# Kernel tuning notes

Hardware: AMD Instinct MI355X
Metric: run time of the kernel (lower is better)

## Reference

```python
import jax, jax.numpy as jnp
import numpy as np
from jax import lax

B, DIM, H, W = 32, 64, 1, 8192
HEADS = 8
EPS_LN = 1e-5
EPS_NORM = 1e-12


def setup_inputs() -> dict:
    key = jax.random.key(0)
    ks = jax.random.split(key, 20)
    g = lambda i, shape, s=0.05: jax.random.normal(ks[i], shape, jnp.float32) * s
    return dict(
        x=jax.random.normal(ks[0], (B, DIM, H, W), jnp.float32),
        qkv_w=g(1, (3 * DIM, DIM)), qkv_b=g(2, (3 * DIM,)),
        dw_w=g(3, (3 * DIM, 1, 3, 3)), dw_b=g(4, (3 * DIM,)),
        proj_w=g(5, (DIM, DIM)), proj_b=g(6, (DIM,)),
        temperature=jnp.ones((HEADS, 1, 1), jnp.float32),
        sp_w=g(7, (DIM,)), sp_b=g(8, (1,)),
        up_w=g(9, (3,)), up_b=g(10, (3,)),
        c2_w=g(11, (1, 1, 2)), c2_b=g(11, (1,)), ln2_w=jnp.ones((W,), jnp.float32), ln2_b=jnp.zeros((W,), jnp.float32),
        c4_w=g(12, (1, 1, 4)), c4_b=g(13, (1,)), ln4_w=jnp.ones((W,), jnp.float32), ln4_b=jnp.zeros((W,), jnp.float32),
        c6_w=g(14, (1, 1, 6)), c6_b=g(15, (1,)), ln6_w=jnp.ones((W,), jnp.float32), ln6_b=jnp.zeros((W,), jnp.float32),
        mp_w=g(16, (DIM,)), mp_b=g(17, (DIM,)),
    )


def _mtl(xs, cw, cb, lw, lb):
    """Multiscale_Temporal_Layer: conv1d 'same' -> LayerNorm(W) -> ELU -> mean pool. xs: (b,1,w)."""
    k = cw.shape[-1]
    tot = k - 1
    lo = tot // 2  # torch 'same': extra pad goes to the right
    y = lax.conv_general_dilated(xs, cw, (1,), [(lo, tot - lo)],
                                 dimension_numbers=('NCH', 'OIH', 'NCH'))
    y = y + cb[None, :, None]
    mu = jnp.mean(y, -1, keepdims=True)
    var = jnp.mean((y - mu) ** 2, -1, keepdims=True)
    y = (y - mu) / jnp.sqrt(var + EPS_LN) * lw + lb
    y = jax.nn.elu(y)
    return jnp.mean(y, -1, keepdims=True)  # (b,1,1)


def _forward(x, qkv_w, qkv_b, dw_w, dw_b, proj_w, proj_b, temperature,
             sp_w, sp_b, up_w, up_b,
             c2_w, c2_b, ln2_w, ln2_b,
             c4_w, c4_b, ln4_w, ln4_b,
             c6_w, c6_b, ln6_w, ln6_b,
             mp_w, mp_b):
    b, c, h, w = x.shape
    hd = c // HEADS  # per-head channel dim
    # 1x1 conv qkv, then depthwise 3x3 conv
    qkv = jnp.einsum('oc,bchw->bohw', qkv_w, x) + qkv_b[None, :, None, None]
    qkv = lax.conv_general_dilated(qkv, dw_w, (1, 1), [(1, 1), (1, 1)],
                                   dimension_numbers=('NCHW', 'OIHW', 'NCHW'),
                                   feature_group_count=3 * c)
    qkv = qkv + dw_b[None, :, None, None]
    q, k, v = jnp.split(qkv, 3, axis=1)
    # Multiscale_Temporal_Attention on v: v is (b,c,1,w)
    xseq = (jnp.einsum('c,bcw->bw', sp_w, v[:, :, 0, :]) + sp_b)[:, None, :]  # (b,1,w)
    up = up_w[None, :, None] * xseq + up_b[None, :, None]  # (b,3,w)
    xx, yy, zz = up[:, 0:1], up[:, 1:2], up[:, 2:3]
    mout = (_mtl(xx, c2_w, c2_b, ln2_w, ln2_b) * xx
            + _mtl(yy, c4_w, c4_b, ln4_w, ln4_b) * yy
            + _mtl(zz, c6_w, c6_b, ln6_w, ln6_b) * zz)  # (b,1,w)
    v = mp_w[None, :, None] * mout + mp_b[None, :, None]  # (b,c,w) via 1x1 conv broadcast
    # channel (transposed) attention over n = h*w tokens
    n = h * w
    q = q.reshape(b, HEADS, hd, n)
    k = k.reshape(b, HEADS, hd, n)
    v = v.reshape(b, HEADS, hd, n)
    q = q / jnp.maximum(jnp.linalg.norm(q, axis=-1, keepdims=True), EPS_NORM)
    k = k / jnp.maximum(jnp.linalg.norm(k, axis=-1, keepdims=True), EPS_NORM)
    attn = jnp.einsum('bhcn,bhdn->bhcd', q, k) * temperature  # (b,heads,hd,hd)
    attn = jax.nn.softmax(attn, axis=-1)
    out = jnp.einsum('bhcd,bhdn->bhcn', attn, v).reshape(b, c, h, w)
    out = jnp.einsum('oc,bchw->bohw', proj_w, out) + proj_b[None, :, None, None]
    return out  # dropouts are identity in eval mode


def reference(x, qkv_w, qkv_b, dw_w, dw_b, proj_w, proj_b, temperature,
              sp_w, sp_b, up_w, up_b,
              c2_w, c2_b, ln2_w, ln2_b,
              c4_w, c4_b, ln4_w, ln4_b,
              c6_w, c6_b, ln6_w, ln6_b,
              mp_w, mp_b):
    return _forward(x, qkv_w, qkv_b, dw_w, dw_b, proj_w, proj_b, temperature,
                    sp_w, sp_b, up_w, up_b,
                    c2_w, c2_b, ln2_w, ln2_b,
                    c4_w, c4_b, ln4_w, ln4_b,
                    c6_w, c6_b, ln6_w, ln6_b,
                    mp_w, mp_b)
```

## Files before the change

kernel.cpp:

```cpp
#include <hip/hip_runtime.h>
#include <hip/hip_bf16.h>
#include <math.h>

#define Wd 8192
#define Bd 32
#define Ttile 64

#define OFF_G    0
#define OFF_H    192
#define OFF_BASE 195
#define OFF_XSEQ 256
#define OFF_PART (256 + Bd*Wd)
#define OFF_S    (OFF_PART + Bd*128*640)
#define OFF_M    (OFF_S + Bd*640)
#define OFF_E    (OFF_M + 96)
#define OFF_F    (OFF_E + Bd*64)
#define OFF_FRAG (OFF_F + Bd*64)

typedef __attribute__((ext_vector_type(8))) short bf16x8;
typedef __attribute__((ext_vector_type(4))) float f32x4;

__device__ __forceinline__ unsigned short f2bf(float v) {
    return __builtin_bit_cast(unsigned short, __float2bfloat16(v));
}
__device__ __forceinline__ float bf2f(unsigned short h) {
    return __builtin_bit_cast(float, (unsigned)h << 16);
}
__device__ __forceinline__ void split2(float v0, float v1, unsigned& hw, unsigned& lw) {
    unsigned short h0 = f2bf(v0), h1 = f2bf(v1);
    unsigned short l0 = f2bf(v0 - bf2f(h0)), l1 = f2bf(v1 - bf2f(h1));
    hw = (unsigned)h0 | ((unsigned)h1 << 16);
    lw = (unsigned)l0 | ((unsigned)l1 << 16);
}
__device__ __forceinline__ unsigned pk2(float v0, float v1) {
    return (unsigned)f2bf(v0) | ((unsigned)f2bf(v1) << 16);
}

__global__ __launch_bounds__(256) void k0_setup(const float* __restrict__ qkv_w,
                         const float* __restrict__ qkv_b,
                         const float* __restrict__ dw_w, const float* __restrict__ dw_b,
                         const float* __restrict__ sp_w, const float* __restrict__ sp_b,
                         float* __restrict__ ws)
{
    int tid = threadIdx.x;
    if (tid < 192) {
        int j = tid >> 6, ch = tid & 63;
        float acc = 0.f;
        for (int c = 0; c < 64; c++)
            acc += sp_w[c] * dw_w[(128+c)*9 + 3 + j] * qkv_w[(128+c)*64 + ch];
        ws[OFF_G + j*64 + ch] = acc;
    } else if (tid < 195) {
        int j = tid - 192;
        float h = 0.f;
        for (int c = 0; c < 64; c++)
            h += sp_w[c] * dw_w[(128+c)*9 + 3 + j] * qkv_b[128+c];
        ws[OFF_H + j] = h;
    } else if (tid == 195) {
        float base = sp_b[0];
        for (int c = 0; c < 64; c++) base += sp_w[c] * dw_b[128+c];
        ws[OFF_BASE] = base;
    }
    __syncthreads();
    for (int it = tid; it < 36*64; it += 256) {
        int lane = it & 63;
        int cidx = it >> 6;
        int ver = cidx / 18;
        int rem = cidx - ver*18;
        int nt = rem >> 1, kb = rem & 1;
        int row = nt*16 + (lane & 15);
        int ks  = kb*32 + (lane >> 4)*8;
        unsigned short u[8];
        #pragma unroll
        for (int e = 0; e < 8; e++) {
            int k = ks + e;
            float v = 0.f;
            if (row < 128)      v = qkv_w[row*64 + k];
            else if (row < 131) v = ws[OFF_G + (row-128)*64 + k];
            unsigned short h = f2bf(v);
            if (ver == 0) u[e] = h;
            else          u[e] = f2bf(v - bf2f(h));
        }
        unsigned* dst = (unsigned*)(ws + OFF_FRAG) + (ver*1152 + (nt*2+kb)*64 + lane)*4;
        dst[0] = (unsigned)u[0] | ((unsigned)u[1] << 16);
        dst[1] = (unsigned)u[2] | ((unsigned)u[3] << 16);
        dst[2] = (unsigned)u[4] | ((unsigned)u[5] << 16);
        dst[3] = (unsigned)u[6] | ((unsigned)u[7] << 16);
    }
}

#define XT_HI 0
#define XT_LO 10752
#define QKH   21504
#define ZLDS  37888
#define SMEM_BYTES (37888 + 1024)

__global__ __launch_bounds__(256, 4) void k1_main(const float* __restrict__ x,
    const float* __restrict__ qkv_b, const float* __restrict__ dw_w,
    const float* __restrict__ dw_b, float* __restrict__ ws)
{
    __shared__ __align__(16) unsigned char smem[SMEM_BYTES];
    const int tid = threadIdx.x, lane = tid & 63, wv = tid >> 6;
    const int g = lane >> 4, lr = lane & 15;
    const int tile = blockIdx.x, b = blockIdx.y;
    const int w0 = tile * Ttile;
    const float* xb = x + (size_t)b * 64 * Wd;
    const bool safe = (tile != 0) && (tile != 127);

    for (int i = tid; i < 672; i += 256) {
        int j = i >> 5, chp = i & 31;
        int pos0 = w0 - 4 + 4*j;
        float4 a, c;
        if (safe || (unsigned)pos0 < (unsigned)Wd) {
            a = *(const float4*)(xb + (size_t)(2*chp)*Wd + pos0);
            c = *(const float4*)(xb + (size_t)(2*chp+1)*Wd + pos0);
        } else {
            a = (float4){0,0,0,0}; c = (float4){0,0,0,0};
        }
        #pragma unroll
        for (int e = 0; e < 4; e++) {
            int row = 4*j + e;
            float va = ((const float*)&a)[e], vc = ((const float*)&c)[e];
            unsigned hw, lw;
            split2(va, vc, hw, lw);
            int boff = row*128 + ((((chp>>2) ^ (row & 7)) << 4) | ((chp & 3) << 2));
            *(unsigned*)(smem + XT_HI + boff) = hw;
            *(unsigned*)(smem + XT_LO + boff) = lw;
        }
    }
    __syncthreads();

    f32x4 acc[3][5];
    #pragma unroll
    for (int i = 0; i < 3; i++)
        #pragma unroll
        for (int m = 0; m < 5; m++) acc[i][m] = (f32x4){0.f,0.f,0.f,0.f};
    const uint4* fragbase = (const uint4*)(ws + OFF_FRAG);

    #pragma unroll
    for (int kb = 0; kb < 2; kb++) {
        bf16x8 axh[5], axl[5];
        #pragma unroll
        for (int mt = 0; mt < 5; mt++) {
            int row = mt*16 + lr + 3;
            int gran = (kb*4 + g) ^ (row & 7);
            axh[mt] = *(const bf16x8*)(smem + XT_HI + row*128 + gran*16);
            axl[mt] = *(const bf16x8*)(smem + XT_LO + row*128 + gran*16);
        }
        #pragma unroll
        for (int nti = 0; nti < 3; nti++) {
            if (nti < 2 || wv == 0) {
                int nt = (nti == 2) ? 8 : (wv + nti*4);
                bf16x8 bh = __builtin_bit_cast(bf16x8, fragbase[(nt*2+kb)*64 + lane]);
                bf16x8 bl = __builtin_bit_cast(bf16x8, fragbase[1152 + (nt*2+kb)*64 + lane]);
                #pragma unroll
                for (int mt = 0; mt < 5; mt++) {
                    acc[nti][mt] = __builtin_amdgcn_mfma_f32_16x16x32_bf16(axh[mt], bh, acc[nti][mt], 0,0,0);
                    acc[nti][mt] = __builtin_amdgcn_mfma_f32_16x16x32_bf16(axl[mt], bh, acc[nti][mt], 0,0,0);
                    acc[nti][mt] = __builtin_amdgcn_mfma_f32_16x16x32_bf16(axh[mt], bl, acc[nti][mt], 0,0,0);
                }
            }
        }
    }

    float* zlds = (float*)(smem + ZLDS);
    #pragma unroll
    for (int nti = 0; nti < 3; nti++) {
        if (!(nti < 2 || wv == 0)) continue;
        int nt = (nti == 2) ? 8 : (wv + nti*4);
        int row = nt*16 + lr;
        if (nt == 8) {
            if (lr < 3) {
                #pragma unroll
                for (int mt = 0; mt < 5; mt++) {
                    float4 vz = { acc[2][mt][0], acc[2][mt][1], acc[2][mt][2], acc[2][mt][3] };
                    *(float4*)(zlds + lr*84 + mt*16 + g*4) = vz;
                }
            }
        } else {
            float bias = qkv_b[row];
            float tb = dw_b[row];
            float t0 = dw_w[row*9+3], t1 = dw_w[row*9+4], t2 = dw_w[row*9+5];
            float4 v[5];
            #pragma unroll
            for (int mt = 0; mt < 5; mt++) {
                #pragma unroll
                for (int r = 0; r < 4; r++) {
                    float val = acc[nti][mt][r] + bias;
                    if (!safe) {
                        int pos = w0 - 1 + mt*16 + g*4 + r;
                        if (pos < 0 || pos >= Wd) val = 0.f;
                    }
                    ((float*)&v[mt])[r] = val;
                }
            }
            int src = (lane + 16) & 63;
            #pragma unroll
            for (int mt = 0; mt < 4; mt++) {
                float a0 = __shfl(v[mt].x,   src), b0 = __shfl(v[mt+1].x, src);
                float a1 = __shfl(v[mt].y,   src), b1 = __shfl(v[mt+1].y, src);
                float in4 = (lane < 48) ? a0 : b0;
                float in5 = (lane < 48) ? a1 : b1;
                float o0 = tb + t0*v[mt].x + t1*v[mt].y + t2*v[mt].z;
                float o1 = tb + t0*v[mt].y + t1*v[mt].z + t2*v[mt].w;
                float o2 = tb + t0*v[mt].z + t1*v[mt].w + t2*in4;
                float o3 = tb + t0*v[mt].w + t1*in4     + t2*in5;
                uint2 hw;
                hw.x = pk2(o0, o1);
                hw.y = pk2(o2, o3);
                int gran = (2*mt + (g>>1)) ^ (row & 7);
                int boff = row*128 + (gran << 4) + ((g & 1) << 3);
                *(uint2*)(smem + QKH + boff) = hw;
            }
        }
    }

    if (tid < 64) {
        float a = ws[OFF_BASE];
        #pragma unroll
        for (int j = 0; j < 3; j++) {
            int wg = w0 + tid + j - 1;
            a += zlds[j*84 + tid + j];
            if (wg >= 0 && wg < Wd) a += ws[OFF_H + j];
        }
        ws[OFF_XSEQ + (size_t)b*Wd + w0 + tid] = a;
    }

    {
        const int rq = wv*16 + lr;
        const int rk = 64 + wv*16 + lr;
        f32x4 sqk = (f32x4){0,0,0,0}, sqq = (f32x4){0,0,0,0}, skk = (f32x4){0,0,0,0};
        #pragma unroll
        for (int kb = 0; kb < 2; kb++) {
            int gran = (kb*4 + g) ^ (lr & 7);
            bf16x8 qh = *(const bf16x8*)(smem + QKH + rq*128 + gran*16);
            bf16x8 kh = *(const bf16x8*)(smem + QKH + rk*128 + gran*16);
            sqk = __builtin_amdgcn_mfma_f32_16x16x32_bf16(qh, kh, sqk, 0,0,0);
            sqq = __builtin_amdgcn_mfma_f32_16x16x32_bf16(qh, qh, sqq, 0,0,0);
            skk = __builtin_amdgcn_mfma_f32_16x16x32_bf16(kh, kh, skk, 0,0,0);
        }
        float* pb = ws + OFF_PART + (size_t)(b*128 + tile)*640;
        int hh = lr >> 3, c2 = lr & 7;
        if (hh == (g >> 1)) {
            #pragma unroll
            for (int r = 0; r < 4; r++) {
                int c1 = (g & 1)*4 + r;
                pb[(2*wv + hh)*64 + c1*8 + c2] = sqk[r];
            }
        }
        if ((lr >> 2) == g) {
            int r = lr & 3;
            pb[512 + wv*16 + lr] = sqq[r];
            pb[576 + wv*16 + lr] = skk[r];
        }
    }
}

__device__ __forceinline__ float blk_reduce_256(float v, float* sc) {
    #pragma unroll
    for (int off = 32; off > 0; off >>= 1) v += __shfl_down(v, off, 64);
    __syncthreads();
    if ((threadIdx.x & 63) == 0) sc[threadIdx.x >> 6] = v;
    __syncthreads();
    return sc[0] + sc[1] + sc[2] + sc[3];
}

__global__ __launch_bounds__(256) void k23(const float* __restrict__ ws,
    const float* __restrict__ up_w, const float* __restrict__ up_b,
    const float* __restrict__ c2_w, const float* __restrict__ c2_b,
    const float* __restrict__ ln2_w, const float* __restrict__ ln2_b,
    const float* __restrict__ c4_w, const float* __restrict__ c4_b,
    const float* __restrict__ ln4_w, const float* __restrict__ ln4_b,
    const float* __restrict__ c6_w, const float* __restrict__ c6_b,
    const float* __restrict__ ln6_w, const float* __restrict__ ln6_b,
    float* __restrict__ wsS, float* __restrict__ wsM)
{
    __shared__ float ys[Wd];
    __shared__ float sc[4];
    int bx = blockIdx.x;
    if (bx < 32) {
        int b = bx;
        const float* part = ws + OFF_PART + (size_t)b*128*640;
        #pragma unroll
        for (int k = 0; k < 3; k++) {
            int idx = threadIdx.x + k*256;
            if (idx < 640) {
                float s0 = 0.f, s1 = 0.f, s2 = 0.f, s3 = 0.f;
                for (int t = 0; t < 128; t += 4) {
                    s0 += part[(size_t)(t  )*640 + idx];
                    s1 += part[(size_t)(t+1)*640 + idx];
                    s2 += part[(size_t)(t+2)*640 + idx];
                    s3 += part[(size_t)(t+3)*640 + idx];
                }
                wsS[b*640 + idx] = (s0 + s1) + (s2 + s3);
            }
        }
        return;
    }
    int t2 = bx - 32;
    int br = t2 / 32, b = t2 % 32;
    const float *cw, *lw, *lb; float cb; int K, lo;
    if (br == 0)      { cw = c2_w; cb = c2_b[0]; lw = ln2_w; lb = ln2_b; K = 2; lo = 0; }
    else if (br == 1) { cw = c4_w; cb = c4_b[0]; lw = ln4_w; lb = ln4_b; K = 4; lo = 1; }
    else              { cw = c6_w; cb = c6_b[0]; lw = ln6_w; lb = ln6_b; K = 6; lo = 2; }
    float uw = up_w[br], ub = up_b[br];
    const float* xr = ws + OFF_XSEQ + (size_t)b*Wd;

    float s = 0.f, s2 = 0.f;
    for (int w = threadIdx.x; w < Wd; w += 256) {
        float y = cb;
        for (int m = 0; m < K; m++) {
            int p = w + m - lo;
            if (p >= 0 && p < Wd) y += cw[m] * (uw*xr[p] + ub);
        }
        ys[w] = y; s += y; s2 += y*y;
    }
    float mu = blk_reduce_256(s, sc) * (1.f/Wd);
    __syncthreads();
    float Ey2 = blk_reduce_256(s2, sc) * (1.f/Wd);
    float var = fmaxf(Ey2 - mu*mu, 0.f);
    float inv = 1.f / sqrtf(var + 1e-5f);
    float se = 0.f;
    for (int w = threadIdx.x; w < Wd; w += 256) {
        float tt = (ys[w]-mu)*inv*lw[w] + lb[w];
        se += (tt > 0.f) ? tt : expm1f(tt);
    }
    float m = blk_reduce_256(se, sc) * (1.f/Wd);
    if (threadIdx.x == 0) wsM[b*3 + br] = m;
}

__global__ __launch_bounds__(256) void k45(const float* __restrict__ ws,
    const float* __restrict__ temperature,
    const float* __restrict__ mp_w, const float* __restrict__ mp_b,
    const float* __restrict__ up_w, const float* __restrict__ up_b,
    const float* __restrict__ proj_w, const float* __restrict__ proj_b,
    float* __restrict__ out)
{
    __shared__ float snk[64], sal[64], sbe[64], sE[64], sF[64];
    const int tid = threadIdx.x;
    const int chunk = blockIdx.x, b = blockIdx.y;
    const float* Sb = ws + OFF_S + b*640;
    float nq = 0.f;
    if (tid < 64) {
        nq = fmaxf(sqrtf(Sb[512 + tid]), 1e-12f);
        snk[tid] = fmaxf(sqrtf(Sb[576 + tid]), 1e-12f);
    }
    __syncthreads();
    if (tid < 64) {
        int h = tid >> 3;
        float temp = temperature[h];
        float lg[8], mx = -1e30f;
        #pragma unroll
        for (int d = 0; d < 8; d++) {
            lg[d] = Sb[8*tid + d] / (nq * snk[h*8 + d]) * temp;
            mx = fmaxf(mx, lg[d]);
        }
        float sum = 0.f;
        #pragma unroll
        for (int d = 0; d < 8; d++) { lg[d] = expf(lg[d] - mx); sum += lg[d]; }
        float a = 0.f, bb = 0.f;
        #pragma unroll
        for (int d = 0; d < 8; d++) {
            float at = lg[d] / sum;
            a  += at * mp_w[h*8 + d];
            bb += at * mp_b[h*8 + d];
        }
        sal[tid] = a; sbe[tid] = bb;
    }
    __syncthreads();
    if (tid < 64) {
        const float* wm = ws + OFF_M + b*3;
        float m2 = wm[0], m4 = wm[1], m6 = wm[2];
        float A = m2*up_w[0] + m4*up_w[1] + m6*up_w[2];
        float C = m2*up_b[0] + m4*up_b[1] + m6*up_b[2];
        float Pa = 0.f, Pb = 0.f;
        for (int c = 0; c < 64; c++) {
            float pw = proj_w[tid*64 + c];
            Pa += pw * sal[c];
            Pb += pw * sbe[c];
        }
        sE[tid] = A * Pa;
        sF[tid] = C * Pa + Pb + proj_b[tid];
    }
    __syncthreads();
    const float4* xs4 = (const float4*)(ws + OFF_XSEQ + (size_t)b*Wd);
    float4 xv = xs4[chunk*128 + (tid & 127)];
    int ohalf = tid >> 7;
    float4* ob = (float4*)out + (size_t)b*64*2048 + chunk*128 + (tid & 127);
    #pragma unroll 8
    for (int oo = 0; oo < 32; oo++) {
        int o = ohalf*32 + oo;
        float e = sE[o], f = sF[o];
        float4 r = { e*xv.x + f, e*xv.y + f, e*xv.z + f, e*xv.w + f };
        ob[(size_t)o*2048] = r;
    }
}

extern "C" void kernel_launch(void* const* d_in, const int* in_sizes, int n_in,
                              void* d_out, int out_size, void* d_ws, size_t ws_size,
                              hipStream_t stream) {
    const float* x      = (const float*)d_in[0];
    const float* qkv_w  = (const float*)d_in[1];
    const float* qkv_b  = (const float*)d_in[2];
    const float* dw_w   = (const float*)d_in[3];
    const float* dw_b   = (const float*)d_in[4];
    const float* proj_w = (const float*)d_in[5];
    const float* proj_b = (const float*)d_in[6];
    const float* temperature = (const float*)d_in[7];
    const float* sp_w   = (const float*)d_in[8];
    const float* sp_b   = (const float*)d_in[9];
    const float* up_w   = (const float*)d_in[10];
    const float* up_b   = (const float*)d_in[11];
    const float* c2_w   = (const float*)d_in[12];
    const float* c2_b   = (const float*)d_in[13];
    const float* ln2_w  = (const float*)d_in[14];
    const float* ln2_b  = (const float*)d_in[15];
    const float* c4_w   = (const float*)d_in[16];
    const float* c4_b   = (const float*)d_in[17];
    const float* ln4_w  = (const float*)d_in[18];
    const float* ln4_b  = (const float*)d_in[19];
    const float* c6_w   = (const float*)d_in[20];
    const float* c6_b   = (const float*)d_in[21];
    const float* ln6_w  = (const float*)d_in[22];
    const float* ln6_b  = (const float*)d_in[23];
    const float* mp_w   = (const float*)d_in[24];
    const float* mp_b   = (const float*)d_in[25];
    float* ws  = (float*)d_ws;
    float* out = (float*)d_out;

    k0_setup<<<1, 256, 0, stream>>>(qkv_w, qkv_b, dw_w, dw_b, sp_w, sp_b, ws);
    k1_main<<<dim3(128, 32), 256, 0, stream>>>(x, qkv_b, dw_w, dw_b, ws);
    k23<<<128, 256, 0, stream>>>(ws, up_w, up_b,
        c2_w, c2_b, ln2_w, ln2_b, c4_w, c4_b, ln4_w, ln4_b, c6_w, c6_b, ln6_w, ln6_b,
        ws + OFF_S, ws + OFF_M);
    k45<<<dim3(16, 32), 256, 0, stream>>>(ws, temperature, mp_w, mp_b,
        up_w, up_b, proj_w, proj_b, out);
}
```

Measured before the change: 126.2 us.

## Drop x low-part split, rebalance z MFMA, split reduction and coefficient kernels

The x tile is now stored only as a single bf16 high part, which halves LDS use and removes one of the three MFMA passes, and the launch bound rises to 5 blocks per SM. The z-column MFMA work is spread across all four waves instead of sitting on wave 0, and LDS is reused for the q/k output after an extra barrier. The partial-sum reduction in k23 is split into 160 blocks, and the per-batch softmax/projection coefficients move into a separate small kernel so the output kernel no longer recomputes them per chunk. Dropping the x low part lowers the accuracy of the qkv projection, and the extra kernel launch adds fixed overhead.

```diff
diff --git a/kernel.cpp b/kernel.cpp
--- a/kernel.cpp
+++ b/kernel.cpp
@@ -25,12 +25,6 @@
 }
 __device__ __forceinline__ float bf2f(unsigned short h) {
     return __builtin_bit_cast(float, (unsigned)h << 16);
-}
-__device__ __forceinline__ void split2(float v0, float v1, unsigned& hw, unsigned& lw) {
-    unsigned short h0 = f2bf(v0), h1 = f2bf(v1);
-    unsigned short l0 = f2bf(v0 - bf2f(h0)), l1 = f2bf(v1 - bf2f(h1));
-    hw = (unsigned)h0 | ((unsigned)h1 << 16);
-    lw = (unsigned)l0 | ((unsigned)l1 << 16);
 }
 __device__ __forceinline__ unsigned pk2(float v0, float v1) {
     return (unsigned)f2bf(v0) | ((unsigned)f2bf(v1) << 16);
@@ -88,13 +82,12 @@
     }
 }
 
-#define XT_HI 0
-#define XT_LO 10752
-#define QKH   21504
-#define ZLDS  37888
-#define SMEM_BYTES (37888 + 1024)
-
-__global__ __launch_bounds__(256, 4) void k1_main(const float* __restrict__ x,
+#define XT    0
+#define QKH   0
+#define ZLDS  16384
+#define SMEM_BYTES (16384 + 1024)
+
+__global__ __launch_bounds__(256, 5) void k1_main(const float* __restrict__ x,
     const float* __restrict__ qkv_b, const float* __restrict__ dw_w,
     const float* __restrict__ dw_b, float* __restrict__ ws)
 {
@@ -119,100 +112,108 @@
         #pragma unroll
         for (int e = 0; e < 4; e++) {
             int row = 4*j + e;
-            float va = ((const float*)&a)[e], vc = ((const float*)&c)[e];
-            unsigned hw, lw;
-            split2(va, vc, hw, lw);
+            unsigned hw = pk2(((const float*)&a)[e], ((const float*)&c)[e]);
             int boff = row*128 + ((((chp>>2) ^ (row & 7)) << 4) | ((chp & 3) << 2));
-            *(unsigned*)(smem + XT_HI + boff) = hw;
-            *(unsigned*)(smem + XT_LO + boff) = lw;
-        }
-    }
-    __syncthreads();
-
-    f32x4 acc[3][5];
-    #pragma unroll
-    for (int i = 0; i < 3; i++)
+            *(unsigned*)(smem + XT + boff) = hw;
+        }
+    }
+    __syncthreads();
+
+    f32x4 acc[2][5];
+    f32x4 accz[2];
+    #pragma unroll
+    for (int i = 0; i < 2; i++) {
+        accz[i] = (f32x4){0.f,0.f,0.f,0.f};
         #pragma unroll
         for (int m = 0; m < 5; m++) acc[i][m] = (f32x4){0.f,0.f,0.f,0.f};
+    }
     const uint4* fragbase = (const uint4*)(ws + OFF_FRAG);
 
     #pragma unroll
     for (int kb = 0; kb < 2; kb++) {
-        bf16x8 axh[5], axl[5];
+        bf16x8 axh[5];
         #pragma unroll
         for (int mt = 0; mt < 5; mt++) {
             int row = mt*16 + lr + 3;
             int gran = (kb*4 + g) ^ (row & 7);
-            axh[mt] = *(const bf16x8*)(smem + XT_HI + row*128 + gran*16);
-            axl[mt] = *(const bf16x8*)(smem + XT_LO + row*128 + gran*16);
-        }
-        #pragma unroll
-        for (int nti = 0; nti < 3; nti++) {
-            if (nti < 2 || wv == 0) {
-                int nt = (nti == 2) ? 8 : (wv + nti*4);
-                bf16x8 bh = __builtin_bit_cast(bf16x8, fragbase[(nt*2+kb)*64 + lane]);
-                bf16x8 bl = __builtin_bit_cast(bf16x8, fragbase[1152 + (nt*2+kb)*64 + lane]);
-                #pragma unroll
-                for (int mt = 0; mt < 5; mt++) {
-                    acc[nti][mt] = __builtin_amdgcn_mfma_f32_16x16x32_bf16(axh[mt], bh, acc[nti][mt], 0,0,0);
-                    acc[nti][mt] = __builtin_amdgcn_mfma_f32_16x16x32_bf16(axl[mt], bh, acc[nti][mt], 0,0,0);
-                    acc[nti][mt] = __builtin_amdgcn_mfma_f32_16x16x32_bf16(axh[mt], bl, acc[nti][mt], 0,0,0);
-                }
-            }
-        }
-    }
-
-    float* zlds = (float*)(smem + ZLDS);
-    #pragma unroll
-    for (int nti = 0; nti < 3; nti++) {
-        if (!(nti < 2 || wv == 0)) continue;
-        int nt = (nti == 2) ? 8 : (wv + nti*4);
-        int row = nt*16 + lr;
-        if (nt == 8) {
-            if (lr < 3) {
-                #pragma unroll
-                for (int mt = 0; mt < 5; mt++) {
-                    float4 vz = { acc[2][mt][0], acc[2][mt][1], acc[2][mt][2], acc[2][mt][3] };
-                    *(float4*)(zlds + lr*84 + mt*16 + g*4) = vz;
-                }
-            }
-        } else {
-            float bias = qkv_b[row];
-            float tb = dw_b[row];
-            float t0 = dw_w[row*9+3], t1 = dw_w[row*9+4], t2 = dw_w[row*9+5];
-            float4 v[5];
+            axh[mt] = *(const bf16x8*)(smem + XT + row*128 + gran*16);
+        }
+        #pragma unroll
+        for (int nti = 0; nti < 2; nti++) {
+            int nt = wv + nti*4;
+            bf16x8 bh = __builtin_bit_cast(bf16x8, fragbase[(nt*2+kb)*64 + lane]);
+            bf16x8 bl = __builtin_bit_cast(bf16x8, fragbase[1152 + (nt*2+kb)*64 + lane]);
             #pragma unroll
             for (int mt = 0; mt < 5; mt++) {
-                #pragma unroll
-                for (int r = 0; r < 4; r++) {
-                    float val = acc[nti][mt][r] + bias;
-                    if (!safe) {
-                        int pos = w0 - 1 + mt*16 + g*4 + r;
-                        if (pos < 0 || pos >= Wd) val = 0.f;
-                    }
-                    ((float*)&v[mt])[r] = val;
+                acc[nti][mt] = __builtin_amdgcn_mfma_f32_16x16x32_bf16(axh[mt], bh, acc[nti][mt], 0,0,0);
+                acc[nti][mt] = __builtin_amdgcn_mfma_f32_16x16x32_bf16(axh[mt], bl, acc[nti][mt], 0,0,0);
+            }
+        }
+        {
+            bf16x8 bzh = __builtin_bit_cast(bf16x8, fragbase[(16+kb)*64 + lane]);
+            bf16x8 bzl = __builtin_bit_cast(bf16x8, fragbase[1152 + (16+kb)*64 + lane]);
+            int rowz = wv*16 + lr + 3;
+            int granz = (kb*4 + g) ^ (rowz & 7);
+            bf16x8 azh = *(const bf16x8*)(smem + XT + rowz*128 + granz*16);
+            accz[0] = __builtin_amdgcn_mfma_f32_16x16x32_bf16(azh, bzh, accz[0], 0,0,0);
+            accz[0] = __builtin_amdgcn_mfma_f32_16x16x32_bf16(azh, bzl, accz[0], 0,0,0);
+            if (wv == 0) {
+                accz[1] = __builtin_amdgcn_mfma_f32_16x16x32_bf16(axh[4], bzh, accz[1], 0,0,0);
+                accz[1] = __builtin_amdgcn_mfma_f32_16x16x32_bf16(axh[4], bzl, accz[1], 0,0,0);
+            }
+        }
+    }
+    __syncthreads();
+
+    float* zlds = (float*)(smem + ZLDS);
+    #pragma unroll
+    for (int nti = 0; nti < 2; nti++) {
+        int nt = wv + nti*4;
+        int row = nt*16 + lr;
+        float bias = qkv_b[row];
+        float tb = dw_b[row];
+        float t0 = dw_w[row*9+3], t1 = dw_w[row*9+4], t2 = dw_w[row*9+5];
+        float4 v[5];
+        #pragma unroll
+        for (int mt = 0; mt < 5; mt++) {
+            #pragma unroll
+            for (int r = 0; r < 4; r++) {
+                float val = acc[nti][mt][r] + bias;
+                if (!safe) {
+                    int pos = w0 - 1 + mt*16 + g*4 + r;
+                    if (pos < 0 || pos >= Wd) val = 0.f;
                 }
+                ((float*)&v[mt])[r] = val;
             }
-            int src = (lane + 16) & 63;
-            #pragma unroll
-            for (int mt = 0; mt < 4; mt++) {
-                float a0 = __shfl(v[mt].x,   src), b0 = __shfl(v[mt+1].x, src);
-                float a1 = __shfl(v[mt].y,   src), b1 = __shfl(v[mt+1].y, src);
-                float in4 = (lane < 48) ? a0 : b0;
-                float in5 = (lane < 48) ? a1 : b1;
-                float o0 = tb + t0*v[mt].x + t1*v[mt].y + t2*v[mt].z;
-                float o1 = tb + t0*v[mt].y + t1*v[mt].z + t2*v[mt].w;
-                float o2 = tb + t0*v[mt].z + t1*v[mt].w + t2*in4;
-                float o3 = tb + t0*v[mt].w + t1*in4     + t2*in5;
-                uint2 hw;
-                hw.x = pk2(o0, o1);
-                hw.y = pk2(o2, o3);
-                int gran = (2*mt + (g>>1)) ^ (row & 7);
-                int boff = row*128 + (gran << 4) + ((g & 1) << 3);
-                *(uint2*)(smem + QKH + boff) = hw;
-            }
-        }
-    }
+        }
+        int src = (lane + 16) & 63;
+        #pragma unroll
+        for (int mt = 0; mt < 4; mt++) {
+            float a0 = __shfl(v[mt].x,   src), b0 = __shfl(v[mt+1].x, src);
+            float a1 = __shfl(v[mt].y,   src), b1 = __shfl(v[mt+1].y, src);
+            float in4 = (lane < 48) ? a0 : b0;
+            float in5 = (lane < 48) ? a1 : b1;
+            float o0 = tb + t0*v[mt].x + t1*v[mt].y + t2*v[mt].z;
+            float o1 = tb + t0*v[mt].y + t1*v[mt].z + t2*v[mt].w;
+            float o2 = tb + t0*v[mt].z + t1*v[mt].w + t2*in4;
+            float o3 = tb + t0*v[mt].w + t1*in4     + t2*in5;
+            uint2 hw;
+            hw.x = pk2(o0, o1);
+            hw.y = pk2(o2, o3);
+            int gran = (2*mt + (g>>1)) ^ (row & 7);
+            int boff = row*128 + (gran << 4) + ((g & 1) << 3);
+            *(uint2*)(smem + QKH + boff) = hw;
+        }
+    }
+    if (lr < 3) {
+        float4 vz0 = { accz[0][0], accz[0][1], accz[0][2], accz[0][3] };
+        *(float4*)(zlds + lr*84 + wv*16 + g*4) = vz0;
+        if (wv == 0) {
+            float4 vz1 = { accz[1][0], accz[1][1], accz[1][2], accz[1][3] };
+            *(float4*)(zlds + lr*84 + 64 + g*4) = vz1;
+        }
+    }
+    __syncthreads();
 
     if (tid < 64) {
         float a = ws[OFF_BASE];
@@ -277,27 +278,27 @@
     __shared__ float ys[Wd];
     __shared__ float sc[4];
     int bx = blockIdx.x;
-    if (bx < 32) {
-        int b = bx;
-        const float* part = ws + OFF_PART + (size_t)b*128*640;
-        #pragma unroll
-        for (int k = 0; k < 3; k++) {
-            int idx = threadIdx.x + k*256;
-            if (idx < 640) {
-                float s0 = 0.f, s1 = 0.f, s2 = 0.f, s3 = 0.f;
-                for (int t = 0; t < 128; t += 4) {
-                    s0 += part[(size_t)(t  )*640 + idx];
-                    s1 += part[(size_t)(t+1)*640 + idx];
-                    s2 += part[(size_t)(t+2)*640 + idx];
-                    s3 += part[(size_t)(t+3)*640 + idx];
-                }
-                wsS[b*640 + idx] = (s0 + s1) + (s2 + s3);
-            }
-        }
+    if (bx < 160) {
+        int b = bx / 5, chunk = bx - (bx/5)*5;
+        int idx = chunk*128 + (threadIdx.x & 127);
+        int half = threadIdx.x >> 7;
+        const float* part = ws + OFF_PART + (size_t)b*128*640 + idx;
+        float s0 = 0.f, s1 = 0.f, s2 = 0.f, s3 = 0.f;
+        int t0 = half*64;
+        for (int t = t0; t < t0 + 64; t += 4) {
+            s0 += part[(size_t)(t  )*640];
+            s1 += part[(size_t)(t+1)*640];
+            s2 += part[(size_t)(t+2)*640];
+            s3 += part[(size_t)(t+3)*640];
+        }
+        float s = (s0 + s1) + (s2 + s3);
+        if (half) ys[threadIdx.x & 127] = s;
+        __syncthreads();
+        if (!half) wsS[b*640 + idx] = s + ys[threadIdx.x];
         return;
     }
-    int t2 = bx - 32;
-    int br = t2 / 32, b = t2 % 32;
+    int t2 = bx - 160;
+    int br = t2 >> 5, b = t2 & 31;
     const float *cw, *lw, *lb; float cb; int K, lo;
     if (br == 0)      { cw = c2_w; cb = c2_b[0]; lw = ln2_w; lb = ln2_b; K = 2; lo = 0; }
     else if (br == 1) { cw = c4_w; cb = c4_b[0]; lw = ln4_w; lb = ln4_b; K = 4; lo = 1; }
@@ -328,58 +329,63 @@
     if (threadIdx.x == 0) wsM[b*3 + br] = m;
 }
 
-__global__ __launch_bounds__(256) void k45(const float* __restrict__ ws,
+__global__ __launch_bounds__(64) void k4_coeffs(const float* __restrict__ ws,
     const float* __restrict__ temperature,
     const float* __restrict__ mp_w, const float* __restrict__ mp_b,
     const float* __restrict__ up_w, const float* __restrict__ up_b,
     const float* __restrict__ proj_w, const float* __restrict__ proj_b,
-    float* __restrict__ out)
+    float* __restrict__ wsE, float* __restrict__ wsF)
 {
-    __shared__ float snk[64], sal[64], sbe[64], sE[64], sF[64];
+    __shared__ float nk[64], alpha[64], beta[64];
+    int b = blockIdx.x, t = threadIdx.x;
+    const float* Sb = ws + OFF_S + b*640;
+    float nq_t = fmaxf(sqrtf(Sb[512 + t]), 1e-12f);
+    nk[t]      = fmaxf(sqrtf(Sb[576 + t]), 1e-12f);
+    __syncthreads();
+    int h = t >> 3;
+    float temp = temperature[h];
+    float lg[8];
+    float mx = -1e30f;
+    #pragma unroll
+    for (int d = 0; d < 8; d++) {
+        lg[d] = Sb[8*t + d] / (nq_t * nk[h*8 + d]) * temp;
+        mx = fmaxf(mx, lg[d]);
+    }
+    float sum = 0.f;
+    #pragma unroll
+    for (int d = 0; d < 8; d++) { lg[d] = expf(lg[d] - mx); sum += lg[d]; }
+    float a = 0.f, bb = 0.f;
+    #pragma unroll
+    for (int d = 0; d < 8; d++) {
+        float at = lg[d] / sum;
+        a  += at * mp_w[h*8 + d];
+        bb += at * mp_b[h*8 + d];
+    }
+    alpha[t] = a; beta[t] = bb;
+    __syncthreads();
+    const float* wm = ws + OFF_M + b*3;
+    float m2 = wm[0], m4 = wm[1], m6 = wm[2];
+    float A = m2*up_w[0] + m4*up_w[1] + m6*up_w[2];
+    float C = m2*up_b[0] + m4*up_b[1] + m6*up_b[2];
+    float Pa = 0.f, Pb = 0.f;
+    for (int c = 0; c < 64; c++) {
+        float pw = proj_w[t*64 + c];
+        Pa += pw * alpha[c];
+        Pb += pw * beta[c];
+    }
+    wsE[b*64 + t] = A * Pa;
+    wsF[b*64 + t] = C * Pa + Pb + proj_b[t];
+}
+
+__global__ __launch_bounds__(256) void k5_out(const float* __restrict__ ws,
+                                              float* __restrict__ out)
+{
+    __shared__ float sE[64], sF[64];
     const int tid = threadIdx.x;
     const int chunk = blockIdx.x, b = blockIdx.y;
-    const float* Sb = ws + OFF_S + b*640;
-    float nq = 0.f;
     if (tid < 64) {
-        nq = fmaxf(sqrtf(Sb[512 + tid]), 1e-12f);
-        snk[tid] = fmaxf(sqrtf(Sb[576 + tid]), 1e-12f);
-    }
-    __syncthreads();
-    if (tid < 64) {
-        int h = tid >> 3;
-        float temp = temperature[h];
-        float lg[8], mx = -1e30f;
-        #pragma unroll
-        for (int d = 0; d < 8; d++) {
-            lg[d] = Sb[8*tid + d] / (nq * snk[h*8 + d]) * temp;
-            mx = fmaxf(mx, lg[d]);
-        }
-        float sum = 0.f;
-        #pragma unroll
-        for (int d = 0; d < 8; d++) { lg[d] = expf(lg[d] - mx); sum += lg[d]; }
-        float a = 0.f, bb = 0.f;
-        #pragma unroll
-        for (int d = 0; d < 8; d++) {
-            float at = lg[d] / sum;
-            a  += at * mp_w[h*8 + d];
-            bb += at * mp_b[h*8 + d];
-        }
-        sal[tid] = a; sbe[tid] = bb;
-    }
-    __syncthreads();
-    if (tid < 64) {
-        const float* wm = ws + OFF_M + b*3;
-        float m2 = wm[0], m4 = wm[1], m6 = wm[2];
-        float A = m2*up_w[0] + m4*up_w[1] + m6*up_w[2];
-        float C = m2*up_b[0] + m4*up_b[1] + m6*up_b[2];
-        float Pa = 0.f, Pb = 0.f;
-        for (int c = 0; c < 64; c++) {
-            float pw = proj_w[tid*64 + c];
-            Pa += pw * sal[c];
-            Pb += pw * sbe[c];
-        }
-        sE[tid] = A * Pa;
-        sF[tid] = C * Pa + Pb + proj_b[tid];
+        sE[tid] = ws[OFF_E + b*64 + tid];
+        sF[tid] = ws[OFF_F + b*64 + tid];
     }
     __syncthreads();
     const float4* xs4 = (const float4*)(ws + OFF_XSEQ + (size_t)b*Wd);
@@ -429,9 +435,10 @@
 
     k0_setup<<<1, 256, 0, stream>>>(qkv_w, qkv_b, dw_w, dw_b, sp_w, sp_b, ws);
     k1_main<<<dim3(128, 32), 256, 0, stream>>>(x, qkv_b, dw_w, dw_b, ws);
-    k23<<<128, 256, 0, stream>>>(ws, up_w, up_b,
+    k23<<<256, 256, 0, stream>>>(ws, up_w, up_b,
         c2_w, c2_b, ln2_w, ln2_b, c4_w, c4_b, ln4_w, ln4_b, c6_w, c6_b, ln6_w, ln6_b,
         ws + OFF_S, ws + OFF_M);
-    k45<<<dim3(16, 32), 256, 0, stream>>>(ws, temperature, mp_w, mp_b,
-        up_w, up_b, proj_w, proj_b, out);
-}
+    k4_coeffs<<<32, 64, 0, stream>>>(ws, temperature, mp_w, mp_b,
+        up_w, up_b, proj_w, proj_b, ws + OFF_E, ws + OFF_F);
+    k5_out<<<dim3(16, 32), 256, 0, stream>>>(ws, out);
+}
```

Result: slower. 130.5 us (+3.4%).
